# Kernel tuning notes

Measured on AMD Instinct MI355X. Metric: run time of the kernel, lower is better.

The kernel has to match this reference:

```python
import jax, jax.numpy as jnp
import numpy as np

# H36M 17-joint skeleton: parent-of array
_PARENTS = [-1, 0, 1, 2, 0, 4, 5, 0, 7, 8, 9, 8, 11, 12, 8, 14, 15]

def _make_triplets():
    # (jp, j, jc) for every joint j with a parent jp and child jc
    trips = []
    for jc, j in enumerate(_PARENTS):
        if j <= 0 and j != 0:
            continue
        if j == -1:
            continue
        jp = _PARENTS[j]
        if jp == -1:
            continue
        trips.append((jp, j, jc))
    return trips

TRIPLETS = _make_triplets()  # 12 fixed triplets

B, N, J, C = 16, 243, 17, 512
H, D = 8, C // 8
EPS = 1e-5


def setup_inputs() -> dict:
    key = jax.random.key(0)
    ks = jax.random.split(key, 5)
    s = 1.0 / np.sqrt(C)
    x = jax.random.normal(ks[0], (B, N, J, C), dtype=jnp.float32)
    Wqkv = jax.random.normal(ks[1], (C, 3 * C), dtype=jnp.float32) * s
    bqkv = jax.random.normal(ks[2], (3 * C,), dtype=jnp.float32) * 0.01
    Wproj = jax.random.normal(ks[3], (C, C), dtype=jnp.float32) * s
    bproj = jax.random.normal(ks[4], (C,), dtype=jnp.float32) * 0.01
    return {"x": x, "Wqkv": Wqkv, "bqkv": bqkv, "Wproj": Wproj, "bproj": bproj}


def _hsdm(x, Wqkv, bqkv, Wproj, bproj):
    # x: (B, N, J, C) -> tokens over joints per frame
    xf = x.reshape(B * N, J, C)
    qkv = xf @ Wqkv + bqkv                                   # (BN, J, 3C)
    qkv = qkv.reshape(B * N, J, 3, H, D).transpose(2, 0, 3, 1, 4)  # (3, BN, H, J, D)
    q, k, v = qkv[0], qkv[1], qkv[2]
    scale = 1.0 / jnp.sqrt(jnp.float32(D))
    attn = jax.nn.softmax(jnp.einsum('bhqd,bhkd->bhqk', q, k) * scale, axis=-1)
    # sequential hierarchical adjustment over fixed skeleton triplets
    # (order matters: later triplets read entries written by earlier ones)
    for jp, j, jc in TRIPLETS:
        half = attn[:, :, j, jp] * 0.5
        attn = attn.at[:, :, j, jc].add(half).at[:, :, jc, j].add(half)
    # dropout is identity at inference
    xa = jnp.einsum('bhqk,bhkd->bhqd', attn, v)              # (BN, H, J, D)
    xa = xa.transpose(0, 2, 1, 3).reshape(B * N, J, C)
    xa = xa @ Wproj + bproj
    y = x + xa.reshape(B, N, J, C)
    mu = jnp.mean(y, axis=-1, keepdims=True)
    var = jnp.var(y, axis=-1, keepdims=True)
    return (y - mu) / jnp.sqrt(var + EPS)                     # LN without affine


def reference(x, Wqkv, bqkv, Wproj, bproj):
    return _hsdm(x, Wqkv, bqkv, Wproj, bproj)
```

## Files before the change

### kernel.cpp

```cpp
#include <hip/hip_runtime.h>

typedef unsigned short u16;
typedef unsigned int u32;
typedef short bf16x8 __attribute__((ext_vector_type(8)));
typedef float f32x4 __attribute__((ext_vector_type(4)));

#define M_ROWS   66096
#define M_PAD    66176
#define C_DIM    512
#define NQKV     1536
#define NFRAME   3888


__device__ __forceinline__ u16 f2bf(float f) {
    u32 u = __float_as_uint(f);
    u32 r = (u + 0x7fffu + ((u >> 16) & 1u)) >> 16;
    return (u16)r;
}
__device__ __forceinline__ float bf2f(u16 v) {
    return __uint_as_float(((u32)v) << 16);
}
__device__ __forceinline__ void async16(const void* g, void* l) {
    __builtin_amdgcn_global_load_lds(
        (const __attribute__((address_space(1))) unsigned int*)g,
        (__attribute__((address_space(3))) unsigned int*)l, 16, 0, 0);
}


__global__ __launch_bounds__(256) void cast_x(const float* __restrict__ x, u16* __restrict__ xb) {
    u32 cid = blockIdx.x * 256u + threadIdx.x;
    u32 m  = cid >> 6;
    u32 c0 = (cid & 63u) * 8u;
    if (m >= M_PAD) return;
    u16 v[8];
    if (m < M_ROWS) {
        const float* p = x + (size_t)m * C_DIM + c0;
        float4 f1 = *(const float4*)p;
        float4 f2 = *(const float4*)(p + 4);
        v[0]=f2bf(f1.x); v[1]=f2bf(f1.y); v[2]=f2bf(f1.z); v[3]=f2bf(f1.w);
        v[4]=f2bf(f2.x); v[5]=f2bf(f2.y); v[6]=f2bf(f2.z); v[7]=f2bf(f2.w);
    } else {
        #pragma unroll
        for (int i = 0; i < 8; ++i) v[i] = 0;
    }
    u16* dst = xb + ((size_t)(c0 >> 5) * M_PAD + m) * 32 + (c0 & 31u);
    *(uint4*)dst = *(const uint4*)v;
}


__global__ __launch_bounds__(256) void cast_w(const float* __restrict__ W, u16* __restrict__ out, int N) {
    __shared__ float tile[32 * 65];
    const int n0 = blockIdx.x * 64;
    const int kt = blockIdx.y;
    const int t  = threadIdx.x;
    for (int i = t; i < 2048; i += 256) {
        int k = i >> 6, n = i & 63;
        tile[k * 65 + n] = W[(size_t)(kt * 32 + k) * N + n0 + n];
    }
    __syncthreads();
    {
        int n = t >> 2, kk0 = (t & 3) * 8;
        u16 v[8];
        #pragma unroll
        for (int j = 0; j < 8; ++j) v[j] = f2bf(tile[(kk0 + j) * 65 + n]);
        u16* dst = out + ((size_t)kt * N + n0 + n) * 32 + kk0;
        *(uint4*)dst = *(const uint4*)v;
    }
}


__global__ __launch_bounds__(256) void gemm1(const u16* __restrict__ xb,
                                             const u16* __restrict__ wt,
                                             const float* __restrict__ bqkv,
                                             u16* __restrict__ qkv) {
    __shared__ u16 As[128 * 32];
    __shared__ u16 Bs[128 * 32];
    __shared__ float biasS[128];

    const int n0 = blockIdx.x * 128;
    const int m0 = blockIdx.y * 128;
    const int t  = threadIdx.x;
    const int w  = t >> 6, l = t & 63;
    const int lr = l & 15, lq = l >> 4;
    const int wr = (w >> 1) * 64, wc = (w & 1) * 64;

    if (t < 128) biasS[t] = bqkv[n0 + t];

    f32x4 acc[4][4] = {};

    for (int kt = 0; kt < 16; ++kt) {
        __syncthreads();
        const u16* ga = xb + ((size_t)kt * M_PAD + m0) * 32;
        const u16* gb = wt + ((size_t)kt * NQKV + n0) * 32;
        async16(ga + (size_t)t * 8,         &As[t * 8]);
        async16(ga + (size_t)(t + 256) * 8, &As[(t + 256) * 8]);
        async16(gb + (size_t)t * 8,         &Bs[t * 8]);
        async16(gb + (size_t)(t + 256) * 8, &Bs[(t + 256) * 8]);
        __syncthreads();

        bf16x8 a[4], b[4];
        #pragma unroll
        for (int i = 0; i < 4; ++i) a[i] = *(const bf16x8*)&As[(wr + i * 16 + lr) * 32 + lq * 8];
        #pragma unroll
        for (int i = 0; i < 4; ++i) b[i] = *(const bf16x8*)&Bs[(wc + i * 16 + lr) * 32 + lq * 8];
        #pragma unroll
        for (int i = 0; i < 4; ++i)
            #pragma unroll
            for (int j = 0; j < 4; ++j)
                acc[i][j] = __builtin_amdgcn_mfma_f32_16x16x32_bf16(a[i], b[j], acc[i][j], 0, 0, 0);
    }

    #pragma unroll
    for (int i = 0; i < 4; ++i) {
        #pragma unroll
        for (int j = 0; j < 4; ++j) {
            const int col  = n0 + wc + j * 16 + lr;
            const float bb = biasS[wc + j * 16 + lr];
            #pragma unroll
            for (int r = 0; r < 4; ++r) {
                const int row = m0 + wr + i * 16 + lq * 4 + r;
                if (row < M_ROWS)
                    qkv[(size_t)row * NQKV + col] = f2bf(acc[i][j][r] + bb);
            }
        }
    }
}


__constant__ int TRJP[13] = {0,1,0,4,0,7,8,7,8,11,7,8,14};
__constant__ int TRJ [13] = {1,2,4,5,7,8,9,8,11,12,8,14,15};
__constant__ int TRJC[13] = {2,3,5,6,8,9,10,11,12,13,14,15,16};

__device__ __forceinline__ float dot8(uint4 qa, uint4 kb) {
    const u32* qu = (const u32*)&qa;
    const u32* ku = (const u32*)&kb;
    float s = 0.f;
    #pragma unroll
    for (int i = 0; i < 4; ++i) {
        float q0 = __uint_as_float(qu[i] << 16);
        float q1 = __uint_as_float(qu[i] & 0xffff0000u);
        float k0 = __uint_as_float(ku[i] << 16);
        float k1 = __uint_as_float(ku[i] & 0xffff0000u);
        s = fmaf(q0, k0, s);
        s = fmaf(q1, k1, s);
    }
    return s;
}

#define QKROW 1552

__global__ __launch_bounds__(256) void attn_k(const u16* __restrict__ qkv, u16* __restrict__ xa) {
    __shared__ u16 qk[17 * QKROW];
    __shared__ float S[4][17 * 18];

    const int f = blockIdx.x;
    const int t = threadIdx.x;
    const int w = t >> 6, l = t & 63;
    const u16* src = qkv + (size_t)f * 17 * NQKV;

    for (int i = t; i < 3264; i += 256) {
        int r = i / 192, c = i - r * 192;
        *(uint4*)&qk[r * QKROW + c * 8] = *(const uint4*)&src[i * 8];
    }
    __syncthreads();

    for (int hh = 0; hh < 2; ++hh) {
        const int h = hh * 4 + w;
        float* Sw = S[w];

        for (int e = l; e < 289; e += 64) {
            int qi = e / 17, ki = e - qi * 17;
            const u16* qp = &qk[qi * QKROW + h * 64];
            const u16* kp = &qk[ki * QKROW + 512 + h * 64];
            float d = 0.f;
            #pragma unroll
            for (int c = 0; c < 8; ++c)
                d += dot8(*(const uint4*)&qp[c * 8], *(const uint4*)&kp[c * 8]);
            Sw[qi * 18 + ki] = d * 0.125f;
        }
        __syncthreads();

        if (l < 17) {
            float mx = -1e30f;
            #pragma unroll
            for (int k = 0; k < 17; ++k) mx = fmaxf(mx, Sw[l * 18 + k]);
            float s = 0.f;
            #pragma unroll
            for (int k = 0; k < 17; ++k) {
                float e = __expf(Sw[l * 18 + k] - mx);
                Sw[l * 18 + k] = e;
                s += e;
            }
            float inv = 1.f / s;
            #pragma unroll
            for (int k = 0; k < 17; ++k) Sw[l * 18 + k] *= inv;
        }
        __syncthreads();

        if (l == 0) {
            #pragma unroll
            for (int tr = 0; tr < 13; ++tr) {
                int jp = TRJP[tr], j = TRJ[tr], jc = TRJC[tr];
                float half = Sw[j * 18 + jp] * 0.5f;
                Sw[j * 18 + jc] += half;
                Sw[jc * 18 + j] += half;
            }
        }
        __syncthreads();

        float vreg[17];
        #pragma unroll
        for (int k = 0; k < 17; ++k) vreg[k] = bf2f(qk[k * QKROW + 1024 + h * 64 + l]);
        const int col = h * 64 + l;
        u16* dst = xa + ((size_t)(col >> 5) * M_PAD) * 32 + (col & 31);
        #pragma unroll
        for (int j = 0; j < 17; ++j) {
            float o = 0.f;
            #pragma unroll
            for (int k = 0; k < 17; ++k) o = fmaf(Sw[j * 18 + k], vreg[k], o);
            const int row = f * 17 + j;
            dst[(size_t)row * 32] = f2bf(o);
        }
        __syncthreads();
    }
}


__global__ __launch_bounds__(256) void gemm2(const u16* __restrict__ xa,
                                             const u16* __restrict__ wt,
                                             const float* __restrict__ bproj,
                                             const float* __restrict__ x,
                                             float* __restrict__ out) {
    __shared__ u16 As[32 * 32];
    __shared__ u16 Bs[512 * 32];
    __shared__ float biasS[512];
    __shared__ float ssum[32], ssq[32];

    const int m0 = blockIdx.x * 32;
    const int t  = threadIdx.x;
    const int w  = t >> 6, l = t & 63;
    const int lr = l & 15, lq = l >> 4;

    for (int i = t; i < 512; i += 256) biasS[i] = bproj[i];
    if (t < 32) { ssum[t] = 0.f; ssq[t] = 0.f; }

    f32x4 acc[2][8] = {};

    for (int kt = 0; kt < 16; ++kt) {
        __syncthreads();
        const u16* ga = xa + ((size_t)kt * M_PAD + m0) * 32;
        const u16* gb = wt + (size_t)kt * 512 * 32;
        if (t < 128) async16(ga + (size_t)t * 8, &As[t * 8]);
        #pragma unroll
        for (int i = 0; i < 8; ++i)
            async16(gb + (size_t)(t + 256 * i) * 8, &Bs[(t + 256 * i) * 8]);
        __syncthreads();

        bf16x8 a[2], b[8];
        #pragma unroll
        for (int i = 0; i < 2; ++i) a[i] = *(const bf16x8*)&As[(i * 16 + lr) * 32 + lq * 8];
        #pragma unroll
        for (int j = 0; j < 8; ++j) b[j] = *(const bf16x8*)&Bs[((w << 7) + j * 16 + lr) * 32 + lq * 8];
        #pragma unroll
        for (int i = 0; i < 2; ++i)
            #pragma unroll
            for (int j = 0; j < 8; ++j)
                acc[i][j] = __builtin_amdgcn_mfma_f32_16x16x32_bf16(a[i], b[j], acc[i][j], 0, 0, 0);
    }

    #pragma unroll
    for (int i = 0; i < 2; ++i) {
        #pragma unroll
        for (int r = 0; r < 4; ++r) {
            const int row = m0 + i * 16 + lq * 4 + r;
            const bool valid = row < M_ROWS;
            float s = 0.f, sq = 0.f;
            #pragma unroll
            for (int j = 0; j < 8; ++j) {
                const int col = (w << 7) + j * 16 + lr;
                float v = acc[i][j][r] + biasS[col];
                if (valid) v += x[(size_t)row * C_DIM + col];
                acc[i][j][r] = v;
                s += v;
                sq = fmaf(v, v, sq);
            }
            #pragma unroll
            for (int m = 1; m < 16; m <<= 1) {
                s  += __shfl_xor(s, m);
                sq += __shfl_xor(sq, m);
            }
            if (lr == 0) {
                atomicAdd(&ssum[i * 16 + lq * 4 + r], s);
                atomicAdd(&ssq [i * 16 + lq * 4 + r], sq);
            }
        }
    }
    __syncthreads();

    #pragma unroll
    for (int i = 0; i < 2; ++i) {
        #pragma unroll
        for (int r = 0; r < 4; ++r) {
            const int row = m0 + i * 16 + lq * 4 + r;
            if (row >= M_ROWS) continue;
            const int li = i * 16 + lq * 4 + r;
            const float mean = ssum[li] * (1.f / 512.f);
            const float var  = ssq[li] * (1.f / 512.f) - mean * mean;
            const float rstd = rsqrtf(var + 1e-5f);
            #pragma unroll
            for (int j = 0; j < 8; ++j) {
                const int col = (w << 7) + j * 16 + lr;
                out[(size_t)row * C_DIM + col] = (acc[i][j][r] - mean) * rstd;
            }
        }
    }
}


extern "C" void kernel_launch(void* const* d_in, const int* in_sizes, int n_in,
                              void* d_out, int out_size, void* d_ws, size_t ws_size,
                              hipStream_t stream) {
    const float* x     = (const float*)d_in[0];
    const float* Wqkv  = (const float*)d_in[1];
    const float* bqkv  = (const float*)d_in[2];
    const float* Wproj = (const float*)d_in[3];
    const float* bproj = (const float*)d_in[4];
    float* out = (float*)d_out;

    u16* xb  = (u16*)d_ws;
    u16* wqt = xb  + (size_t)M_PAD * C_DIM;
    u16* wpt = wqt + (size_t)NQKV * C_DIM;
    u16* qkv = wpt + (size_t)C_DIM * C_DIM;
    u16* xa  = qkv + (size_t)M_PAD * NQKV;

    cast_x<<<(M_PAD * 64) / 256, 256, 0, stream>>>(x, xb);
    cast_w<<<dim3(NQKV / 64, 16), 256, 0, stream>>>(Wqkv, wqt, NQKV);
    cast_w<<<dim3(C_DIM / 64, 16), 256, 0, stream>>>(Wproj, wpt, C_DIM);
    gemm1<<<dim3(NQKV / 128, M_PAD / 128), 256, 0, stream>>>(xb, wqt, bqkv, qkv);
    attn_k<<<NFRAME, 256, 0, stream>>>(qkv, xa);
    gemm2<<<(M_ROWS + 31) / 32, 256, 0, stream>>>(xa, wpt, bproj, x, out);
}
```

Measured before the change: 769.0 us.

## Split projection GEMM into square-tiled GEMM plus separate LayerNorm kernel

```diff
diff --git a/kernel.cpp b/kernel.cpp
--- a/kernel.cpp
+++ b/kernel.cpp
@@ -226,94 +226,92 @@
 }
 
 
-__global__ __launch_bounds__(256) void gemm2(const u16* __restrict__ xa,
-                                             const u16* __restrict__ wt,
-                                             const float* __restrict__ bproj,
-                                             const float* __restrict__ x,
-                                             float* __restrict__ out) {
-    __shared__ u16 As[32 * 32];
-    __shared__ u16 Bs[512 * 32];
-    __shared__ float biasS[512];
-    __shared__ float ssum[32], ssq[32];
-
-    const int m0 = blockIdx.x * 32;
+__global__ __launch_bounds__(256) void gemm2_gemm(const u16* __restrict__ xa,
+                                                  const u16* __restrict__ wt,
+                                                  const float* __restrict__ bproj,
+                                                  const float* __restrict__ x,
+                                                  float* __restrict__ y) {
+    __shared__ u16 As[128 * 32];
+    __shared__ u16 Bs[128 * 32];
+    __shared__ float biasS[128];
+
+    const int n0 = blockIdx.x * 128;
+    const int m0 = blockIdx.y * 128;
     const int t  = threadIdx.x;
     const int w  = t >> 6, l = t & 63;
     const int lr = l & 15, lq = l >> 4;
-
-    for (int i = t; i < 512; i += 256) biasS[i] = bproj[i];
-    if (t < 32) { ssum[t] = 0.f; ssq[t] = 0.f; }
-
-    f32x4 acc[2][8] = {};
+    const int wr = (w >> 1) * 64, wc = (w & 1) * 64;
+
+    if (t < 128) biasS[t] = bproj[n0 + t];
+
+    f32x4 acc[4][4] = {};
 
     for (int kt = 0; kt < 16; ++kt) {
         __syncthreads();
         const u16* ga = xa + ((size_t)kt * M_PAD + m0) * 32;
-        const u16* gb = wt + (size_t)kt * 512 * 32;
-        if (t < 128) async16(ga + (size_t)t * 8, &As[t * 8]);
-        #pragma unroll
-        for (int i = 0; i < 8; ++i)
-            async16(gb + (size_t)(t + 256 * i) * 8, &Bs[(t + 256 * i) * 8]);
-        __syncthreads();
-
-        bf16x8 a[2], b[8];
-        #pragma unroll
-        for (int i = 0; i < 2; ++i) a[i] = *(const bf16x8*)&As[(i * 16 + lr) * 32 + lq * 8];
-        #pragma unroll
-        for (int j = 0; j < 8; ++j) b[j] = *(const bf16x8*)&Bs[((w << 7) + j * 16 + lr) * 32 + lq * 8];
-        #pragma unroll
-        for (int i = 0; i < 2; ++i)
-            #pragma unroll
-            for (int j = 0; j < 8; ++j)
+        const u16* gb = wt + ((size_t)kt * C_DIM + n0) * 32;
+        async16(ga + (size_t)t * 8,         &As[t * 8]);
+        async16(ga + (size_t)(t + 256) * 8, &As[(t + 256) * 8]);
+        async16(gb + (size_t)t * 8,         &Bs[t * 8]);
+        async16(gb + (size_t)(t + 256) * 8, &Bs[(t + 256) * 8]);
+        __syncthreads();
+
+        bf16x8 a[4], b[4];
+        #pragma unroll
+        for (int i = 0; i < 4; ++i) a[i] = *(const bf16x8*)&As[(wr + i * 16 + lr) * 32 + lq * 8];
+        #pragma unroll
+        for (int i = 0; i < 4; ++i) b[i] = *(const bf16x8*)&Bs[(wc + i * 16 + lr) * 32 + lq * 8];
+        #pragma unroll
+        for (int i = 0; i < 4; ++i)
+            #pragma unroll
+            for (int j = 0; j < 4; ++j)
                 acc[i][j] = __builtin_amdgcn_mfma_f32_16x16x32_bf16(a[i], b[j], acc[i][j], 0, 0, 0);
     }
 
     #pragma unroll
-    for (int i = 0; i < 2; ++i) {
-        #pragma unroll
-        for (int r = 0; r < 4; ++r) {
-            const int row = m0 + i * 16 + lq * 4 + r;
-            const bool valid = row < M_ROWS;
-            float s = 0.f, sq = 0.f;
-            #pragma unroll
-            for (int j = 0; j < 8; ++j) {
-                const int col = (w << 7) + j * 16 + lr;
-                float v = acc[i][j][r] + biasS[col];
-                if (valid) v += x[(size_t)row * C_DIM + col];
-                acc[i][j][r] = v;
-                s += v;
-                sq = fmaf(v, v, sq);
+    for (int i = 0; i < 4; ++i) {
+        #pragma unroll
+        for (int j = 0; j < 4; ++j) {
+            const int col  = n0 + wc + j * 16 + lr;
+            const float bb = biasS[wc + j * 16 + lr];
+            #pragma unroll
+            for (int r = 0; r < 4; ++r) {
+                const int row = m0 + wr + i * 16 + lq * 4 + r;
+                if (row < M_ROWS) {
+                    const size_t idx = (size_t)row * C_DIM + col;
+                    y[idx] = acc[i][j][r] + bb + x[idx];
+                }
             }
-            #pragma unroll
-            for (int m = 1; m < 16; m <<= 1) {
-                s  += __shfl_xor(s, m);
-                sq += __shfl_xor(sq, m);
-            }
-            if (lr == 0) {
-                atomicAdd(&ssum[i * 16 + lq * 4 + r], s);
-                atomicAdd(&ssq [i * 16 + lq * 4 + r], sq);
-            }
-        }
-    }
-    __syncthreads();
-
+        }
+    }
+}
+
+
+__global__ __launch_bounds__(256) void ln_k(const float* __restrict__ y, float* __restrict__ out) {
+    const int row = blockIdx.x * 4 + (threadIdx.x >> 6);
+    const int l   = threadIdx.x & 63;
+    const float* p = y + (size_t)row * C_DIM + l * 8;
+    float4 a = *(const float4*)p;
+    float4 b = *(const float4*)(p + 4);
+    float s  = a.x + a.y + a.z + a.w + b.x + b.y + b.z + b.w;
+    float sq = a.x*a.x + a.y*a.y + a.z*a.z + a.w*a.w
+             + b.x*b.x + b.y*b.y + b.z*b.z + b.w*b.w;
     #pragma unroll
-    for (int i = 0; i < 2; ++i) {
-        #pragma unroll
-        for (int r = 0; r < 4; ++r) {
-            const int row = m0 + i * 16 + lq * 4 + r;
-            if (row >= M_ROWS) continue;
-            const int li = i * 16 + lq * 4 + r;
-            const float mean = ssum[li] * (1.f / 512.f);
-            const float var  = ssq[li] * (1.f / 512.f) - mean * mean;
-            const float rstd = rsqrtf(var + 1e-5f);
-            #pragma unroll
-            for (int j = 0; j < 8; ++j) {
-                const int col = (w << 7) + j * 16 + lr;
-                out[(size_t)row * C_DIM + col] = (acc[i][j][r] - mean) * rstd;
-            }
-        }
-    }
+    for (int m = 1; m < 64; m <<= 1) {
+        s  += __shfl_xor(s, m);
+        sq += __shfl_xor(sq, m);
+    }
+    const float mean = s * (1.f / 512.f);
+    const float var  = sq * (1.f / 512.f) - mean * mean;
+    const float rstd = rsqrtf(var + 1e-5f);
+    float* q = out + (size_t)row * C_DIM + l * 8;
+    float4 o1, o2;
+    o1.x = (a.x - mean) * rstd; o1.y = (a.y - mean) * rstd;
+    o1.z = (a.z - mean) * rstd; o1.w = (a.w - mean) * rstd;
+    o2.x = (b.x - mean) * rstd; o2.y = (b.y - mean) * rstd;
+    o2.z = (b.z - mean) * rstd; o2.w = (b.w - mean) * rstd;
+    *(float4*)q = o1;
+    *(float4*)(q + 4) = o2;
 }
 
 
@@ -332,11 +330,13 @@
     u16* wpt = wqt + (size_t)NQKV * C_DIM;
     u16* qkv = wpt + (size_t)C_DIM * C_DIM;
     u16* xa  = qkv + (size_t)M_PAD * NQKV;
+    float* y = (float*)qkv;
 
     cast_x<<<(M_PAD * 64) / 256, 256, 0, stream>>>(x, xb);
     cast_w<<<dim3(NQKV / 64, 16), 256, 0, stream>>>(Wqkv, wqt, NQKV);
     cast_w<<<dim3(C_DIM / 64, 16), 256, 0, stream>>>(Wproj, wpt, C_DIM);
     gemm1<<<dim3(NQKV / 128, M_PAD / 128), 256, 0, stream>>>(xb, wqt, bqkv, qkv);
     attn_k<<<NFRAME, 256, 0, stream>>>(qkv, xa);
-    gemm2<<<(M_ROWS + 31) / 32, 256, 0, stream>>>(xa, wpt, bproj, x, out);
-}
+    gemm2_gemm<<<dim3(C_DIM / 128, M_PAD / 128), 256, 0, stream>>>(xa, wpt, bproj, x, y);
+    ln_k<<<M_ROWS / 4, 256, 0, stream>>>(y, out);
+}
```

Measured after the change: 743.8 us. 3.3% less time.
